# Kernel tuning notes

Hardware: AMD Instinct MI355X
Metric: run time of the kernel (lower is better)

Reference implementation:

```python
import jax, jax.numpy as jnp
import numpy as np

N = 50000      # nodes
E = 800000     # edges
F_IN = 128     # in_channels
H = 128        # hidden_channels
C = 10         # num_classes
G = 512        # graphs in batch
EPS = 1e-5     # batchnorm eps


def setup_inputs() -> dict:
    key = jax.random.key(0)
    ks = jax.random.split(key, 18)
    s = 0.05
    return {
        "x": jax.random.normal(ks[0], (N, F_IN), jnp.float32),
        "edge_index": jax.random.randint(ks[1], (2, E), 0, N, dtype=jnp.int32),
        "batch": jnp.sort(jax.random.randint(ks[2], (N,), 0, G, dtype=jnp.int32)),
        "W1": jax.random.normal(ks[3], (F_IN, H), jnp.float32) * s,
        "b1": jnp.zeros((H,), jnp.float32),
        "gamma1": jnp.ones((H,), jnp.float32),
        "beta1": jnp.zeros((H,), jnp.float32),
        "mean1": jax.random.normal(ks[4], (H,), jnp.float32) * 0.1,
        "var1": jax.random.uniform(ks[5], (H,), jnp.float32, 0.5, 1.5),
        "W2": jax.random.normal(ks[6], (H, H), jnp.float32) * s,
        "b2": jnp.zeros((H,), jnp.float32),
        "gamma2": jnp.ones((H,), jnp.float32),
        "beta2": jnp.zeros((H,), jnp.float32),
        "mean2": jax.random.normal(ks[7], (H,), jnp.float32) * 0.1,
        "var2": jax.random.uniform(ks[8], (H,), jnp.float32, 0.5, 1.5),
        "Wlin": jax.random.normal(ks[9], (H, C), jnp.float32) * s,
        "blin": jnp.zeros((C,), jnp.float32),
    }


def _gcn_conv(x, W, b, src, dst):
    # GCNConv with add_self_loops=True, symmetric normalization.
    h = x @ W                                             # [N, H]
    deg = jax.ops.segment_sum(jnp.ones((E,), h.dtype), dst, num_segments=N) + 1.0
    dis = jax.lax.rsqrt(deg)                              # deg^{-1/2}, [N]
    norm = dis[src] * dis[dst]                            # [E]
    agg = jax.ops.segment_sum(h[src] * norm[:, None], dst, num_segments=N)
    agg = agg + h * (dis * dis)[:, None]                  # self-loop term
    return agg + b


def _bn_eval(x, gamma, beta, mean, var):
    return gamma * (x - mean) * jax.lax.rsqrt(var + EPS) + beta


def reference(x, edge_index, batch, W1, b1, gamma1, beta1, mean1, var1,
              W2, b2, gamma2, beta2, mean2, var2, Wlin, blin):
    src, dst = edge_index[0], edge_index[1]
    h = _gcn_conv(x, W1, b1, src, dst)
    h = jax.nn.relu(_bn_eval(h, gamma1, beta1, mean1, var1))
    # dropout: identity in eval mode
    h = _gcn_conv(h, W2, b2, src, dst)
    h = jax.nn.relu(_bn_eval(h, gamma2, beta2, mean2, var2))
    # global_mean_pool over graph ids
    sums = jax.ops.segment_sum(h, batch, num_segments=G)          # [G, H]
    cnts = jax.ops.segment_sum(jnp.ones((N,), h.dtype), batch, num_segments=G)
    pooled = sums / jnp.maximum(cnts, 1.0)[:, None]
    return pooled @ Wlin + blin                                   # [G, C]
```

## Files before the change

kernel.cpp:

```cpp
#include <hip/hip_runtime.h>
#include <hip/hip_bf16.h>

#define N_NODES 50000
#define N_EDGES 800000
#define HDIM 128
#define NGRAPH 512
#define NCLS 10
#define BN_EPS 1e-5f
#define MAXDEG 64

typedef unsigned int  uint32;
typedef unsigned short ushort16;

__device__ inline float2 bf2f(uint32 u) {
    return make_float2(__uint_as_float(u << 16), __uint_as_float(u & 0xffff0000u));
}
__device__ inline ushort16 f2bf(float f) {
    uint32 u = __float_as_uint(f);
    u += 0x7fffu + ((u >> 16) & 1u);
    return (ushort16)(u >> 16);
}
__device__ inline uint32 packbf2(float lo, float hi) {
    return (uint32)f2bf(lo) | ((uint32)f2bf(hi) << 16);
}

__global__ __launch_bounds__(256) void bucket_edges(const int* __restrict__ src,
                                                    const int* __restrict__ dst,
                                                    int* __restrict__ deg,
                                                    int* __restrict__ epad, int ne)
{
    int e = blockIdx.x * 256 + threadIdx.x;
    if (e >= ne) return;
    int d   = dst[e];
    int pos = atomicAdd(&deg[d], 1);
    epad[(size_t)d * MAXDEG + pos] = src[e];
}

__global__ __launch_bounds__(256) void rsqrt_deg(const int* __restrict__ deg,
                                                 float* __restrict__ dis, int n)
{
    int i = blockIdx.x * 256 + threadIdx.x;
    if (i < n) dis[i] = rsqrtf((float)deg[i] + 1.0f);
}

template <typename TIN>
__global__ __launch_bounds__(256) void gemm_nk128(const TIN* __restrict__ X,
                                                  const float* __restrict__ W,
                                                  ushort16* __restrict__ Y, int nrows)
{
    __shared__ float xs[32][36];
    __shared__ float ws[32][128];
    const int t    = threadIdx.x;
    const int row0 = blockIdx.x * 32;
    const int tx   = t & 31;
    const int ty   = t >> 5;

    float acc[4][4];
    #pragma unroll
    for (int i = 0; i < 4; ++i)
        #pragma unroll
        for (int j = 0; j < 4; ++j) acc[i][j] = 0.f;

    const int lr = t >> 3;
    const int lk = (t & 7) << 2;
    const int wr = t >> 5;
    const int wc = (t & 31) << 2;

    for (int k0 = 0; k0 < 128; k0 += 32) {
        float4 xv = make_float4(0.f, 0.f, 0.f, 0.f);
        int grow = row0 + lr;
        if (grow < nrows) {
            const TIN* p = X + (size_t)grow * HDIM + k0 + lk;
            if constexpr (sizeof(TIN) == 4) {
                xv = *(const float4*)p;
            } else {
                uint2 u = *(const uint2*)p;
                float2 a = bf2f(u.x), bb = bf2f(u.y);
                xv = make_float4(a.x, a.y, bb.x, bb.y);
            }
        }
        xs[lr][lk] = xv.x; xs[lr][lk + 1] = xv.y; xs[lr][lk + 2] = xv.z; xs[lr][lk + 3] = xv.w;
        #pragma unroll
        for (int i = 0; i < 4; ++i) {
            int kk = wr + i * 8;
            *(float4*)&ws[kk][wc] = *(const float4*)(W + (size_t)(k0 + kk) * HDIM + wc);
        }
        __syncthreads();
        #pragma unroll
        for (int kk = 0; kk < 32; kk += 4) {
            float4 wv[4];
            #pragma unroll
            for (int j = 0; j < 4; ++j) wv[j] = *(const float4*)&ws[kk + j][tx << 2];
            #pragma unroll
            for (int i = 0; i < 4; ++i) {
                float4 xr = *(const float4*)&xs[ty * 4 + i][kk];
                acc[i][0] += xr.x * wv[0].x; acc[i][1] += xr.x * wv[0].y;
                acc[i][2] += xr.x * wv[0].z; acc[i][3] += xr.x * wv[0].w;
                acc[i][0] += xr.y * wv[1].x; acc[i][1] += xr.y * wv[1].y;
                acc[i][2] += xr.y * wv[1].z; acc[i][3] += xr.y * wv[1].w;
                acc[i][0] += xr.z * wv[2].x; acc[i][1] += xr.z * wv[2].y;
                acc[i][2] += xr.z * wv[2].z; acc[i][3] += xr.z * wv[2].w;
                acc[i][0] += xr.w * wv[3].x; acc[i][1] += xr.w * wv[3].y;
                acc[i][2] += xr.w * wv[3].z; acc[i][3] += xr.w * wv[3].w;
            }
        }
        __syncthreads();
    }
    #pragma unroll
    for (int i = 0; i < 4; ++i) {
        int grow = row0 + ty * 4 + i;
        if (grow < nrows) {
            uint2 o;
            o.x = packbf2(acc[i][0], acc[i][1]);
            o.y = packbf2(acc[i][2], acc[i][3]);
            *(uint2*)(Y + (size_t)grow * HDIM + (tx << 2)) = o;
        }
    }
}

__global__ __launch_bounds__(256) void gather_bn_relu(const ushort16* __restrict__ h,
                                                      const int* __restrict__ epad,
                                                      const int* __restrict__ deg,
                                                      const float* __restrict__ dis,
                                                      const float* __restrict__ b,
                                                      const float* __restrict__ gamma,
                                                      const float* __restrict__ beta,
                                                      const float* __restrict__ mean,
                                                      const float* __restrict__ var,
                                                      ushort16* __restrict__ out, int n)
{
    int node = blockIdx.x * 4 + (threadIdx.x >> 6);
    if (node >= n) return;
    const int lane = threadIdx.x & 63;
    const int q    = lane >> 4;
    const int ci   = (lane & 15) << 3;
    const int cnt_e = deg[node];
    const int base  = node * MAXDEG;
    const float dd  = dis[node];

    int   s_all  = 0;
    float nm_all = 0.f;
    if (lane < cnt_e) {
        s_all  = epad[base + lane];
        nm_all = dis[s_all] * dd;
    }

    float acc[8] = {0.f, 0.f, 0.f, 0.f, 0.f, 0.f, 0.f, 0.f};
    for (int j = q; j < cnt_e; j += 4) {
        int   s  = __shfl(s_all, j);
        float nm = __shfl(nm_all, j);
        uint4 v  = *(const uint4*)(h + (size_t)s * HDIM + ci);
        float2 f0 = bf2f(v.x), f1 = bf2f(v.y), f2 = bf2f(v.z), f3 = bf2f(v.w);
        acc[0] += f0.x * nm; acc[1] += f0.y * nm;
        acc[2] += f1.x * nm; acc[3] += f1.y * nm;
        acc[4] += f2.x * nm; acc[5] += f2.y * nm;
        acc[6] += f3.x * nm; acc[7] += f3.y * nm;
    }
    #pragma unroll
    for (int k = 0; k < 8; ++k) {
        acc[k] += __shfl_xor(acc[k], 16);
        acc[k] += __shfl_xor(acc[k], 32);
    }

    if (q == 0) {
        uint4 hv = *(const uint4*)(h + (size_t)node * HDIM + ci);
        float2 g0 = bf2f(hv.x), g1 = bf2f(hv.y), g2 = bf2f(hv.z), g3 = bf2f(hv.w);
        float dd2 = dd * dd;
        float a[8] = {acc[0] + g0.x * dd2, acc[1] + g0.y * dd2,
                      acc[2] + g1.x * dd2, acc[3] + g1.y * dd2,
                      acc[4] + g2.x * dd2, acc[5] + g2.y * dd2,
                      acc[6] + g3.x * dd2, acc[7] + g3.y * dd2};
        float o[8];
        #pragma unroll
        for (int k = 0; k < 8; ++k) {
            int c = ci + k;
            float sc = gamma[c] * rsqrtf(var[c] + BN_EPS);
            float r  = (a[k] + b[c] - mean[c]) * sc + beta[c];
            o[k] = fmaxf(r, 0.f);
        }
        uint4 ov;
        ov.x = packbf2(o[0], o[1]); ov.y = packbf2(o[2], o[3]);
        ov.z = packbf2(o[4], o[5]); ov.w = packbf2(o[6], o[7]);
        *(uint4*)(out + (size_t)node * HDIM + ci) = ov;
    }
}

__global__ __launch_bounds__(128) void pool_sum(const ushort16* __restrict__ h,
                                                const int* __restrict__ batch,
                                                float* __restrict__ sums,
                                                float* __restrict__ cnt, int n)
{
    int c  = threadIdx.x;
    int n0 = blockIdx.x * 32;
    if (n0 >= n) return;
    int nend = min(n0 + 32, n);
    int curg = batch[n0];
    float acc = 0.f;
    int run = 0;
    for (int i = n0; i < nend; ++i) {
        int g   = batch[i];
        float v = __uint_as_float((uint32)h[(size_t)i * HDIM + c] << 16);
        if (g != curg) {
            atomicAdd(&sums[(size_t)curg * HDIM + c], acc);
            if (c == 0) atomicAdd(&cnt[curg], (float)run);
            acc = 0.f; run = 0; curg = g;
        }
        acc += v; run++;
    }
    atomicAdd(&sums[(size_t)curg * HDIM + c], acc);
    if (c == 0) atomicAdd(&cnt[curg], (float)run);
}

__global__ __launch_bounds__(128) void final_lin(const float* __restrict__ sums,
                                                 const float* __restrict__ cnt,
                                                 const float* __restrict__ Wlin,
                                                 const float* __restrict__ blin,
                                                 float* __restrict__ out)
{
    __shared__ float red[NCLS][2];
    int g = blockIdx.x;
    int t = threadIdx.x;
    float ic = 1.f / fmaxf(cnt[g], 1.f);
    float v  = sums[(size_t)g * HDIM + t] * ic;
    float p[NCLS];
    #pragma unroll
    for (int c = 0; c < NCLS; ++c) p[c] = v * Wlin[t * NCLS + c];
    #pragma unroll
    for (int c = 0; c < NCLS; ++c) {
        float x = p[c];
        for (int off = 32; off > 0; off >>= 1) x += __shfl_down(x, off);
        if ((t & 63) == 0) red[c][t >> 6] = x;
    }
    __syncthreads();
    if (t < NCLS) out[g * NCLS + t] = red[t][0] + red[t][1] + blin[t];
}

extern "C" void kernel_launch(void* const* d_in, const int* in_sizes, int n_in,
                              void* d_out, int out_size, void* d_ws, size_t ws_size,
                              hipStream_t stream)
{
    const float* x     = (const float*)d_in[0];
    const int*   ei    = (const int*)d_in[1];
    const int*   srcp  = ei;
    const int*   dstp  = ei + N_EDGES;
    const int*   batch = (const int*)d_in[2];
    const float* W1    = (const float*)d_in[3];
    const float* b1    = (const float*)d_in[4];
    const float* g1    = (const float*)d_in[5];
    const float* be1   = (const float*)d_in[6];
    const float* m1    = (const float*)d_in[7];
    const float* v1    = (const float*)d_in[8];
    const float* W2    = (const float*)d_in[9];
    const float* b2    = (const float*)d_in[10];
    const float* g2    = (const float*)d_in[11];
    const float* be2   = (const float*)d_in[12];
    const float* m2    = (const float*)d_in[13];
    const float* v2    = (const float*)d_in[14];
    const float* Wlin  = (const float*)d_in[15];
    const float* blin  = (const float*)d_in[16];
    float*       out   = (float*)d_out;

    ushort16* bufA = (ushort16*)d_ws;
    ushort16* bufB = bufA + (size_t)N_NODES * HDIM;
    int*   epad = (int*)(bufB + (size_t)N_NODES * HDIM);
    int*   deg  = epad + (size_t)N_NODES * MAXDEG;
    float* cnt  = (float*)(deg + N_NODES);
    float* sums = cnt + NGRAPH;
    float* dis  = sums + (size_t)NGRAPH * HDIM;

    hipMemsetAsync(deg, 0,
                   (N_NODES + NGRAPH + (size_t)NGRAPH * HDIM) * sizeof(float), stream);

    bucket_edges<<<(N_EDGES + 255) / 256, 256, 0, stream>>>(srcp, dstp, deg, epad, N_EDGES);
    rsqrt_deg<<<(N_NODES + 255) / 256, 256, 0, stream>>>(deg, dis, N_NODES);

    const int gemm_blocks   = (N_NODES + 31) / 32;
    const int gather_blocks = (N_NODES + 3) / 4;

    gemm_nk128<float><<<gemm_blocks, 256, 0, stream>>>(x, W1, bufA, N_NODES);
    gather_bn_relu<<<gather_blocks, 256, 0, stream>>>(bufA, epad, deg, dis,
                                                      b1, g1, be1, m1, v1, bufB, N_NODES);
    gemm_nk128<ushort16><<<gemm_blocks, 256, 0, stream>>>(bufB, W2, bufA, N_NODES);
    gather_bn_relu<<<gather_blocks, 256, 0, stream>>>(bufA, epad, deg, dis,
                                                      b2, g2, be2, m2, v2, bufB, N_NODES);
    pool_sum<<<(N_NODES + 31) / 32, 128, 0, stream>>>(bufB, batch, sums, cnt, N_NODES);
    final_lin<<<NGRAPH, 128, 0, stream>>>(sums, cnt, Wlin, blin, out);
}
```

Before: 300.7 us.

## Fuse front-end kernels, switch to fp16 with MFMA gemm2 and u16 edge lists

Merges GEMM1, edge bucketing and W2 transpose/convert into one launch, and drops the separate rsqrt kernel by recomputing degree normalisation inline in the gather. Switches intermediate storage from bf16 to fp16, stores neighbour ids as 16-bit, and replaces the second GEMM with an MFMA f16 kernel. The gather loop is unrolled by two to keep more loads in flight. These changes aim to cut launch count, memory traffic and GEMM cost, at the risk of fp16 range issues and reliance on node count fitting in 16 bits.

```diff
diff --git a/kernel.cpp b/kernel.cpp
--- a/kernel.cpp
+++ b/kernel.cpp
@@ -1,5 +1,6 @@
 #include <hip/hip_runtime.h>
 #include <hip/hip_bf16.h>
+#include <hip/hip_fp16.h>
 
 #define N_NODES 50000
 #define N_EDGES 800000
@@ -9,51 +10,65 @@
 #define BN_EPS 1e-5f
 #define MAXDEG 64
 
-typedef unsigned int  uint32;
-typedef unsigned short ushort16;
-
-__device__ inline float2 bf2f(uint32 u) {
-    return make_float2(__uint_as_float(u << 16), __uint_as_float(u & 0xffff0000u));
-}
-__device__ inline ushort16 f2bf(float f) {
-    uint32 u = __float_as_uint(f);
-    u += 0x7fffu + ((u >> 16) & 1u);
-    return (ushort16)(u >> 16);
-}
-__device__ inline uint32 packbf2(float lo, float hi) {
-    return (uint32)f2bf(lo) | ((uint32)f2bf(hi) << 16);
-}
-
-__global__ __launch_bounds__(256) void bucket_edges(const int* __restrict__ src,
-                                                    const int* __restrict__ dst,
-                                                    int* __restrict__ deg,
-                                                    int* __restrict__ epad, int ne)
-{
-    int e = blockIdx.x * 256 + threadIdx.x;
-    if (e >= ne) return;
-    int d   = dst[e];
-    int pos = atomicAdd(&deg[d], 1);
-    epad[(size_t)d * MAXDEG + pos] = src[e];
-}
-
-__global__ __launch_bounds__(256) void rsqrt_deg(const int* __restrict__ deg,
-                                                 float* __restrict__ dis, int n)
-{
-    int i = blockIdx.x * 256 + threadIdx.x;
-    if (i < n) dis[i] = rsqrtf((float)deg[i] + 1.0f);
-}
-
-template <typename TIN>
-__global__ __launch_bounds__(256) void gemm_nk128(const TIN* __restrict__ X,
-                                                  const float* __restrict__ W,
-                                                  ushort16* __restrict__ Y, int nrows)
+typedef unsigned int   uint32;
+typedef unsigned short u16;
+typedef __attribute__((ext_vector_type(8))) _Float16 half8;
+typedef __attribute__((ext_vector_type(4))) float f32x4;
+
+__device__ inline u16 f2h(float f) {
+    return __half_as_ushort(__float2half(f));
+}
+__device__ inline float2 h2f2(uint32 u) {
+    __half2 h = *(__half2*)&u;
+    return __half22float2(h);
+}
+__device__ inline uint32 packh2(float lo, float hi) {
+    return (uint32)f2h(lo) | ((uint32)f2h(hi) << 16);
+}
+
+#define GEMM1_BLOCKS 1563
+#define W2T_BLOCKS 8
+#define FRONT_GRID (W2T_BLOCKS + 3 * GEMM1_BLOCKS)
+
+__global__ __launch_bounds__(256) void front(const float* __restrict__ x,
+                                             const float* __restrict__ W1,
+                                             u16* __restrict__ bufA,
+                                             const int* __restrict__ src,
+                                             const int* __restrict__ dst,
+                                             int* __restrict__ deg,
+                                             u16* __restrict__ epad,
+                                             const float* __restrict__ W2,
+                                             u16* __restrict__ W2t)
 {
     __shared__ float xs[32][36];
     __shared__ float ws[32][128];
-    const int t    = threadIdx.x;
-    const int row0 = blockIdx.x * 32;
-    const int tx   = t & 31;
-    const int ty   = t >> 5;
+    const int tid = threadIdx.x;
+    int bid = blockIdx.x;
+
+    if (bid < W2T_BLOCKS) {
+        int t0 = bid * 256 + tid;
+        for (int i = t0; i < HDIM * HDIM; i += W2T_BLOCKS * 256) {
+            int k = i >> 7, n = i & 127;
+            W2t[n * HDIM + k] = f2h(W2[i]);
+        }
+        return;
+    }
+    bid -= W2T_BLOCKS;
+    const int grp = bid / 3, rem = bid % 3;
+
+    if (rem != 0) {
+        int e = (grp * 2 + (rem - 1)) * 256 + tid;
+        if (e < N_EDGES) {
+            int d   = dst[e];
+            int pos = atomicAdd(&deg[d], 1);
+            epad[d * MAXDEG + pos] = (u16)src[e];
+        }
+        return;
+    }
+
+    const int row0 = grp * 32;
+    const int tx   = tid & 31;
+    const int ty   = tid >> 5;
 
     float acc[4][4];
     #pragma unroll
@@ -61,29 +76,20 @@
         #pragma unroll
         for (int j = 0; j < 4; ++j) acc[i][j] = 0.f;
 
-    const int lr = t >> 3;
-    const int lk = (t & 7) << 2;
-    const int wr = t >> 5;
-    const int wc = (t & 31) << 2;
+    const int lr = tid >> 3;
+    const int lk = (tid & 7) << 2;
+    const int wr = tid >> 5;
+    const int wc = (tid & 31) << 2;
 
     for (int k0 = 0; k0 < 128; k0 += 32) {
         float4 xv = make_float4(0.f, 0.f, 0.f, 0.f);
         int grow = row0 + lr;
-        if (grow < nrows) {
-            const TIN* p = X + (size_t)grow * HDIM + k0 + lk;
-            if constexpr (sizeof(TIN) == 4) {
-                xv = *(const float4*)p;
-            } else {
-                uint2 u = *(const uint2*)p;
-                float2 a = bf2f(u.x), bb = bf2f(u.y);
-                xv = make_float4(a.x, a.y, bb.x, bb.y);
-            }
-        }
+        if (grow < N_NODES) xv = *(const float4*)(x + (size_t)grow * HDIM + k0 + lk);
         xs[lr][lk] = xv.x; xs[lr][lk + 1] = xv.y; xs[lr][lk + 2] = xv.z; xs[lr][lk + 3] = xv.w;
         #pragma unroll
         for (int i = 0; i < 4; ++i) {
             int kk = wr + i * 8;
-            *(float4*)&ws[kk][wc] = *(const float4*)(W + (size_t)(k0 + kk) * HDIM + wc);
+            *(float4*)&ws[kk][wc] = *(const float4*)(W1 + (size_t)(k0 + kk) * HDIM + wc);
         }
         __syncthreads();
         #pragma unroll
@@ -109,25 +115,65 @@
     #pragma unroll
     for (int i = 0; i < 4; ++i) {
         int grow = row0 + ty * 4 + i;
-        if (grow < nrows) {
+        if (grow < N_NODES) {
             uint2 o;
-            o.x = packbf2(acc[i][0], acc[i][1]);
-            o.y = packbf2(acc[i][2], acc[i][3]);
-            *(uint2*)(Y + (size_t)grow * HDIM + (tx << 2)) = o;
-        }
-    }
-}
-
-__global__ __launch_bounds__(256) void gather_bn_relu(const ushort16* __restrict__ h,
-                                                      const int* __restrict__ epad,
+            o.x = packh2(acc[i][0], acc[i][1]);
+            o.y = packh2(acc[i][2], acc[i][3]);
+            *(uint2*)(bufA + (size_t)grow * HDIM + (tx << 2)) = o;
+        }
+    }
+}
+
+#define BT_STRIDE 144
+__global__ __launch_bounds__(256) void gemm2_mfma(const u16* __restrict__ A,
+                                                  const u16* __restrict__ W2t,
+                                                  u16* __restrict__ Y, int nrows)
+{
+    __shared__ u16 bt[HDIM * BT_STRIDE];
+    const int tid = threadIdx.x;
+    for (int i = tid; i < HDIM * HDIM / 8; i += 256) {
+        int n  = i >> 4;
+        int k8 = (i & 15) << 3;
+        *(uint4*)&bt[n * BT_STRIDE + k8] = *(const uint4*)&W2t[n * HDIM + k8];
+    }
+    __syncthreads();
+
+    const int wave = tid >> 6, lane = tid & 63;
+    const int rowbase = blockIdx.x * 64 + wave * 16;
+    if (rowbase >= nrows) return;
+    const int n = lane & 15, q = lane >> 4;
+
+    half8 a[4];
+    const u16* arow = A + (size_t)(rowbase + n) * HDIM;
+    #pragma unroll
+    for (int kc = 0; kc < 4; ++kc)
+        a[kc] = *(const half8*)(arow + kc * 32 + q * 8);
+
+    #pragma unroll
+    for (int t = 0; t < 8; ++t) {
+        f32x4 acc = {0.f, 0.f, 0.f, 0.f};
+        #pragma unroll
+        for (int kc = 0; kc < 4; ++kc) {
+            half8 b = *(const half8*)&bt[(t * 16 + n) * BT_STRIDE + kc * 32 + q * 8];
+            acc = __builtin_amdgcn_mfma_f32_16x16x32_f16(a[kc], b, acc, 0, 0, 0);
+        }
+        #pragma unroll
+        for (int r = 0; r < 4; ++r) {
+            int grow = rowbase + q * 4 + r;
+            Y[(size_t)grow * HDIM + t * 16 + n] = f2h(acc[r]);
+        }
+    }
+}
+
+__global__ __launch_bounds__(256) void gather_bn_relu(const u16* __restrict__ h,
+                                                      const u16* __restrict__ epad,
                                                       const int* __restrict__ deg,
-                                                      const float* __restrict__ dis,
                                                       const float* __restrict__ b,
                                                       const float* __restrict__ gamma,
                                                       const float* __restrict__ beta,
                                                       const float* __restrict__ mean,
                                                       const float* __restrict__ var,
-                                                      ushort16* __restrict__ out, int n)
+                                                      u16* __restrict__ out, int n)
 {
     int node = blockIdx.x * 4 + (threadIdx.x >> 6);
     if (node >= n) return;
@@ -135,26 +181,43 @@
     const int q    = lane >> 4;
     const int ci   = (lane & 15) << 3;
     const int cnt_e = deg[node];
-    const int base  = node * MAXDEG;
-    const float dd  = dis[node];
+    const float dd  = rsqrtf((float)cnt_e + 1.0f);
+
+    uint4 hv = *(const uint4*)(h + (size_t)node * HDIM + ci);
 
     int   s_all  = 0;
     float nm_all = 0.f;
     if (lane < cnt_e) {
-        s_all  = epad[base + lane];
-        nm_all = dis[s_all] * dd;
+        s_all  = epad[node * MAXDEG + lane];
+        nm_all = rsqrtf((float)deg[s_all] + 1.0f) * dd;
     }
 
     float acc[8] = {0.f, 0.f, 0.f, 0.f, 0.f, 0.f, 0.f, 0.f};
-    for (int j = q; j < cnt_e; j += 4) {
-        int   s  = __shfl(s_all, j);
-        float nm = __shfl(nm_all, j);
-        uint4 v  = *(const uint4*)(h + (size_t)s * HDIM + ci);
-        float2 f0 = bf2f(v.x), f1 = bf2f(v.y), f2 = bf2f(v.z), f3 = bf2f(v.w);
-        acc[0] += f0.x * nm; acc[1] += f0.y * nm;
-        acc[2] += f1.x * nm; acc[3] += f1.y * nm;
-        acc[4] += f2.x * nm; acc[5] += f2.y * nm;
-        acc[6] += f3.x * nm; acc[7] += f3.y * nm;
+    int j = q;
+    for (; j + 4 < cnt_e; j += 8) {
+        int   s0 = __shfl(s_all, j);     float nm0 = __shfl(nm_all, j);
+        int   s1 = __shfl(s_all, j + 4); float nm1 = __shfl(nm_all, j + 4);
+        uint4 v0 = *(const uint4*)(h + (size_t)s0 * HDIM + ci);
+        uint4 v1 = *(const uint4*)(h + (size_t)s1 * HDIM + ci);
+        float2 f0 = h2f2(v0.x), f1 = h2f2(v0.y), f2 = h2f2(v0.z), f3 = h2f2(v0.w);
+        acc[0] += f0.x * nm0; acc[1] += f0.y * nm0;
+        acc[2] += f1.x * nm0; acc[3] += f1.y * nm0;
+        acc[4] += f2.x * nm0; acc[5] += f2.y * nm0;
+        acc[6] += f3.x * nm0; acc[7] += f3.y * nm0;
+        float2 g0 = h2f2(v1.x), g1 = h2f2(v1.y), g2 = h2f2(v1.z), g3 = h2f2(v1.w);
+        acc[0] += g0.x * nm1; acc[1] += g0.y * nm1;
+        acc[2] += g1.x * nm1; acc[3] += g1.y * nm1;
+        acc[4] += g2.x * nm1; acc[5] += g2.y * nm1;
+        acc[6] += g3.x * nm1; acc[7] += g3.y * nm1;
+    }
+    if (j < cnt_e) {
+        int   s0 = __shfl(s_all, j); float nm0 = __shfl(nm_all, j);
+        uint4 v0 = *(const uint4*)(h + (size_t)s0 * HDIM + ci);
+        float2 f0 = h2f2(v0.x), f1 = h2f2(v0.y), f2 = h2f2(v0.z), f3 = h2f2(v0.w);
+        acc[0] += f0.x * nm0; acc[1] += f0.y * nm0;
+        acc[2] += f1.x * nm0; acc[3] += f1.y * nm0;
+        acc[4] += f2.x * nm0; acc[5] += f2.y * nm0;
+        acc[6] += f3.x * nm0; acc[7] += f3.y * nm0;
     }
     #pragma unroll
     for (int k = 0; k < 8; ++k) {
@@ -163,8 +226,7 @@
     }
 
     if (q == 0) {
-        uint4 hv = *(const uint4*)(h + (size_t)node * HDIM + ci);
-        float2 g0 = bf2f(hv.x), g1 = bf2f(hv.y), g2 = bf2f(hv.z), g3 = bf2f(hv.w);
+        float2 g0 = h2f2(hv.x), g1 = h2f2(hv.y), g2 = h2f2(hv.z), g3 = h2f2(hv.w);
         float dd2 = dd * dd;
         float a[8] = {acc[0] + g0.x * dd2, acc[1] + g0.y * dd2,
                       acc[2] + g1.x * dd2, acc[3] + g1.y * dd2,
@@ -179,13 +241,13 @@
             o[k] = fmaxf(r, 0.f);
         }
         uint4 ov;
-        ov.x = packbf2(o[0], o[1]); ov.y = packbf2(o[2], o[3]);
-        ov.z = packbf2(o[4], o[5]); ov.w = packbf2(o[6], o[7]);
+        ov.x = packh2(o[0], o[1]); ov.y = packh2(o[2], o[3]);
+        ov.z = packh2(o[4], o[5]); ov.w = packh2(o[6], o[7]);
         *(uint4*)(out + (size_t)node * HDIM + ci) = ov;
     }
 }
 
-__global__ __launch_bounds__(128) void pool_sum(const ushort16* __restrict__ h,
+__global__ __launch_bounds__(128) void pool_sum(const u16* __restrict__ h,
                                                 const int* __restrict__ batch,
                                                 float* __restrict__ sums,
                                                 float* __restrict__ cnt, int n)
@@ -199,7 +261,7 @@
     int run = 0;
     for (int i = n0; i < nend; ++i) {
         int g   = batch[i];
-        float v = __uint_as_float((uint32)h[(size_t)i * HDIM + c] << 16);
+        float v = __half2float(__ushort_as_half(h[(size_t)i * HDIM + c]));
         if (g != curg) {
             atomicAdd(&sums[(size_t)curg * HDIM + c], acc);
             if (c == 0) atomicAdd(&cnt[curg], (float)run);
@@ -260,28 +322,25 @@
     const float* blin  = (const float*)d_in[16];
     float*       out   = (float*)d_out;
 
-    ushort16* bufA = (ushort16*)d_ws;
-    ushort16* bufB = bufA + (size_t)N_NODES * HDIM;
-    int*   epad = (int*)(bufB + (size_t)N_NODES * HDIM);
-    int*   deg  = epad + (size_t)N_NODES * MAXDEG;
+    int*   deg  = (int*)d_ws;
     float* cnt  = (float*)(deg + N_NODES);
     float* sums = cnt + NGRAPH;
-    float* dis  = sums + (size_t)NGRAPH * HDIM;
+    u16*   bufA = (u16*)(sums + (size_t)NGRAPH * HDIM);
+    u16*   bufB = bufA + (size_t)N_NODES * HDIM;
+    u16*   epad = bufB + (size_t)N_NODES * HDIM;
+    u16*   W2t  = epad + (size_t)N_NODES * MAXDEG;
 
     hipMemsetAsync(deg, 0,
                    (N_NODES + NGRAPH + (size_t)NGRAPH * HDIM) * sizeof(float), stream);
 
-    bucket_edges<<<(N_EDGES + 255) / 256, 256, 0, stream>>>(srcp, dstp, deg, epad, N_EDGES);
-    rsqrt_deg<<<(N_NODES + 255) / 256, 256, 0, stream>>>(deg, dis, N_NODES);
-
-    const int gemm_blocks   = (N_NODES + 31) / 32;
+    front<<<FRONT_GRID, 256, 0, stream>>>(x, W1, bufA, srcp, dstp, deg, epad, W2, W2t);
+
     const int gather_blocks = (N_NODES + 3) / 4;
 
-    gemm_nk128<float><<<gemm_blocks, 256, 0, stream>>>(x, W1, bufA, N_NODES);
-    gather_bn_relu<<<gather_blocks, 256, 0, stream>>>(bufA, epad, deg, dis,
+    gather_bn_relu<<<gather_blocks, 256, 0, stream>>>(bufA, epad, deg,
                                                       b1, g1, be1, m1, v1, bufB, N_NODES);
-    gemm_nk128<ushort16><<<gemm_blocks, 256, 0, stream>>>(bufB, W2, bufA, N_NODES);
-    gather_bn_relu<<<gather_blocks, 256, 0, stream>>>(bufA, epad, deg, dis,
+    gemm2_mfma<<<(N_NODES + 63) / 64, 256, 0, stream>>>(bufB, W2t, bufA, N_NODES);
+    gather_bn_relu<<<gather_blocks, 256, 0, stream>>>(bufA, epad, deg,
                                                       b2, g2, be2, m2, v2, bufB, N_NODES);
     pool_sum<<<(N_NODES + 31) / 32, 128, 0, stream>>>(bufB, batch, sums, cnt, N_NODES);
     final_lin<<<NGRAPH, 128, 0, stream>>>(sums, cnt, Wlin, blin, out);
```

Measured after the change: 257.3 us. 1.17x faster.
